# Kernel tuning notes

Hardware: AMD Instinct MI355X
Metric: run time of the kernel (lower is better)

## Reference

```python
import jax, jax.numpy as jnp
import numpy as np

NH = 8          # n_heads
EPS = 1e-12     # layer_norm_eps


def _ln(x, g, b, eps=EPS):
    m = x.mean(-1, keepdims=True)
    v = jnp.var(x, axis=-1, keepdims=True)
    return (x - m) / jnp.sqrt(v + eps) * g + b


def _heads(x):
    # [B,S,H] -> [B,NH,S,H/NH]
    B, S, H = x.shape
    return x.reshape(B, S, NH, H // NH).transpose(0, 2, 1, 3)


def setup_inputs() -> dict:
    B, S, H, INNER = 32, 512, 512, 2048
    n_items = 50000
    std = 0.02
    ks = list(jax.random.split(jax.random.key(0), 20))
    inp = {}
    inp['x'] = jax.random.normal(ks[0], (B, S, H), jnp.float32)
    inp['value_input'] = jax.random.normal(ks[1], (B, S, H), jnp.float32)
    inp['beha_emb'] = jax.random.normal(ks[2], (B, S, H), jnp.float32)
    inp['pos_table'] = std * jax.random.normal(ks[3], (S, H), jnp.float32)
    names = ['q', 'k', 'v', 'pk', 'pq', 'bk', 'bq', 'd']
    for i, n in enumerate(names):
        inp['W' + n] = std * jax.random.normal(ks[4 + i], (H, H), jnp.float32)
        inp['b' + n] = jnp.zeros((H,), jnp.float32)
    inp['ln_g'] = jnp.ones((H,), jnp.float32)
    inp['ln_b'] = jnp.zeros((H,), jnp.float32)
    inp['W1'] = std * jax.random.normal(ks[12], (H, INNER), jnp.float32)
    inp['b1'] = jnp.zeros((INNER,), jnp.float32)
    inp['W2'] = std * jax.random.normal(ks[13], (INNER, H), jnp.float32)
    inp['b2'] = jnp.zeros((H,), jnp.float32)
    inp['ln2_g'] = jnp.ones((H,), jnp.float32)
    inp['ln2_b'] = jnp.zeros((H,), jnp.float32)
    inp['item_seq'] = jax.random.randint(ks[14], (B, S), 0, n_items, jnp.int32)
    return inp


def reference(x, value_input, beha_emb, pos_table, Wq, bq, Wk, bk, Wv, bv,
              Wpk, bpk, Wpq, bpq, Wbk, bbk, Wbq, bbq, Wd, bd, ln_g, ln_b,
              W1, b1, W2, b2, ln2_g, ln2_b, item_seq):
    B, S, H = x.shape
    dh = H // NH
    pos = pos_table[:S][None]  # [1,S,H] position_embedding(arange(S))

    q = _heads(x @ Wq + bq)
    k = _heads(x @ Wk + bk)
    v = _heads(value_input @ Wv + bv + value_input)  # value(value_input) + value_input
    pk = _heads(jnp.broadcast_to(pos @ Wpk + bpk, (B, S, H)))
    pq = _heads(jnp.broadcast_to(pos @ Wpq + bpq, (B, S, H)))
    bhk = _heads(beha_emb @ Wbk + bbk)
    bhq = _heads(beha_emb @ Wbq + bbq)

    # disentangled score: q.k^T + q.((beha_k+pos_k)/2)^T + ((beha_q+pos_q)/2).k^T
    scores = (jnp.einsum('bhqd,bhkd->bhqk', q, k)
              + jnp.einsum('bhqd,bhkd->bhqk', q, (bhk + pk) * 0.5)
              + jnp.einsum('bhqd,bhkd->bhqk', (bhq + pq) * 0.5, k))
    scores = scores / (dh ** 0.5)

    # causal + padding mask: (1 - mask) * -10000
    valid = item_seq > 0                              # [B,S]
    causal = jnp.tril(jnp.ones((S, S), bool))         # [S,S]
    ok = valid[:, None, None, :] & causal[None, None]
    scores = scores + jnp.where(ok, 0.0, -10000.0)

    probs = jax.nn.softmax(scores, axis=-1)
    ctx = jnp.einsum('bhqk,bhkd->bhqd', probs, v)
    ctx = ctx.transpose(0, 2, 1, 3).reshape(B, S, H)

    attn_out = _ln(ctx @ Wd + bd + x, ln_g, ln_b)

    # FeedForward (RecBole): dense1 -> gelu -> dense2 -> LN(residual)
    h = jax.nn.gelu(attn_out @ W1 + b1, approximate=False)
    h = h @ W2 + b2
    return _ln(h + attn_out, ln2_g, ln2_b)
```

## Files before the change

### kernel.cpp

```cpp
#include <hip/hip_runtime.h>
#include <math.h>


typedef unsigned short u16;
typedef __attribute__((ext_vector_type(8))) short bf16x8;
typedef __attribute__((ext_vector_type(4))) float f32x4;

#define NM 16384

__device__ __forceinline__ u16 f2b(float f) {
  union { float f; unsigned u; } x; x.f = f;
  return (u16)((x.u + 0x7fffu + ((x.u >> 16) & 1u)) >> 16);
}
__device__ __forceinline__ float b2f(u16 u) {
  union { unsigned u; float f; } x; x.u = ((unsigned)u) << 16; return x.f;
}
__device__ __forceinline__ f32x4 mfma16(bf16x8 a, bf16x8 b, f32x4 c) {
  return __builtin_amdgcn_mfma_f32_16x16x32_bf16(a, b, c, 0, 0, 0);
}
__device__ __forceinline__ void gl16(const u16* g, u16* l) {
  __builtin_amdgcn_global_load_lds(
      (const __attribute__((address_space(1))) unsigned int*)(const void*)g,
      (__attribute__((address_space(3))) unsigned int*)(void*)l, 16, 0, 0);
}
__device__ __forceinline__ bf16x8 baddv(bf16x8 a, bf16x8 b) {
  bf16x8 r;
  #pragma unroll
  for (int e = 0; e < 8; ++e) r[e] = (short)f2b(b2f((u16)a[e]) + b2f((u16)b[e]));
  return r;
}

__device__ __forceinline__ void kloop(
    const u16* __restrict__ A, const u16* __restrict__ W,
    int m0, int n0, int K, int kiters, u16* As, u16* Bs, bool vres,
    f32x4 (&acc)[4][4])
{
  const int tid = threadIdx.x;
  const int wave = tid>>6, lane = tid&63, quad = lane>>4, l16 = lane&15;
  const int wm = wave>>1, wn = wave&1;
  const int r1 = tid>>2;
  const int ch1 = (((tid&3) ^ ((r1>>1)&3)) << 3);
  const int qsw = ((quad ^ ((l16>>1)&3)) << 3);
  const u16* pA = A + (size_t)(m0+r1)*K + ch1;
  const u16* pB = W + (size_t)(n0+r1)*K + ch1;
  u16* sa = As + tid*8;  u16* sb = Bs + tid*8;
  for (int it = 0; it < kiters; ++it) {
    const int k0 = it*32;
    gl16(pA + k0, sa); gl16(pA + (size_t)64*K + k0, sa + 2048);
    gl16(pB + k0, sb); gl16(pB + (size_t)64*K + k0, sb + 2048);
    __syncthreads();
    bf16x8 af[4], bf[4];
    #pragma unroll
    for (int i = 0; i < 4; ++i)
      af[i] = *(const bf16x8*)&As[(wm*64 + i*16 + l16)*32 + qsw];
    #pragma unroll
    for (int j = 0; j < 4; ++j)
      bf[j] = *(const bf16x8*)&Bs[(wn*64 + j*16 + l16)*32 + qsw];
    if (vres) {
      #pragma unroll
      for (int j = 0; j < 4; ++j) {
        const int start = n0 + wn*64 + j*16;
        if ((start & ~31) == k0) {
          const int c = (start & 31) + l16;
          #pragma unroll
          for (int i = 0; i < 4; ++i)
            #pragma unroll
            for (int rr = 0; rr < 4; ++rr) {
              const int rw = wm*64 + i*16 + quad*4 + rr;
              const int sw = ((((c>>3) ^ ((rw>>1)&3)) << 3) | (c & 7));
              acc[i][j][rr] += b2f(As[rw*32 + sw]);
            }
        }
      }
    }
    #pragma unroll
    for (int i = 0; i < 4; ++i)
      #pragma unroll
      for (int j = 0; j < 4; ++j)
        acc[i][j] = mfma16(af[i], bf[j], acc[i][j]);
    __syncthreads();
  }
}

__device__ __forceinline__ void epi_std(
    f32x4 (&acc)[4][4], const float* __restrict__ bias,
    const u16* __restrict__ ex, int exmode, float scale, int gelu,
    u16* __restrict__ out, int m0, int n0, int N, u16* til)
{
  const int tid = threadIdx.x;
  const int wave = tid>>6, lane = tid&63, quad = lane>>4, l16 = lane&15;
  const int wm = wave>>1, wn = wave&1;
  #pragma unroll
  for (int pass = 0; pass < 2; ++pass) {
    if (wm == pass) {
      #pragma unroll
      for (int j = 0; j < 4; ++j) {
        const int c = wn*64 + j*16 + l16;
        const float bv = bias[n0 + c];
        #pragma unroll
        for (int i = 0; i < 4; ++i)
          #pragma unroll
          for (int rr = 0; rr < 4; ++rr) {
            float v = acc[i][j][rr] + bv;
            if (gelu) v = 0.5f*v*(1.0f + erff(v*0.70710678118654752f));
            til[(i*16 + quad*4 + rr)*136 + c] = f2b(v);
          }
      }
    }
    __syncthreads();
    const int r = tid>>2, ck = tid&3;
    const int gr = m0 + pass*64 + r;
    #pragma unroll
    for (int kk = 0; kk < 4; ++kk) {
      const int cc = ck*32 + kk*8, gc = n0 + cc;
      u16 e8[8];
      *(uint4*)e8 = *(const uint4*)&til[r*136 + cc];
      if (exmode) {
        const u16* ep = (exmode == 1) ? &ex[(size_t)(gr & 511)*512 + gc]
                                      : &ex[(size_t)gr*512 + gc];
        #pragma unroll
        for (int e = 0; e < 8; ++e) e8[e] = f2b((b2f(e8[e]) + b2f(ep[e]))*scale);
      } else if (scale != 1.0f) {
        #pragma unroll
        for (int e = 0; e < 8; ++e) e8[e] = f2b(b2f(e8[e])*scale);
      }
      *(uint4*)&out[(size_t)gr*N + gc] = *(uint4*)e8;
    }
    __syncthreads();
  }
}

__device__ __forceinline__ void epi_vt(
    f32x4 (&acc)[4][4], const float* __restrict__ bias,
    u16* __restrict__ Vt, int m0, int n0, u16* til)
{
  const int tid = threadIdx.x;
  const int wave = tid>>6, lane = tid&63, quad = lane>>4, l16 = lane&15;
  const int wm = wave>>1, wn = wave&1;
  const int b = m0 >> 9, s0 = m0 & 511;
  #pragma unroll
  for (int pass = 0; pass < 2; ++pass) {
    if (wn == pass) {
      #pragma unroll
      for (int j = 0; j < 4; ++j) {
        const int cl = j*16 + l16;
        const float bv = bias[n0 + pass*64 + cl];
        #pragma unroll
        for (int i = 0; i < 4; ++i)
          #pragma unroll
          for (int rr = 0; rr < 4; ++rr)
            til[cl*136 + wm*64 + i*16 + quad*4 + rr] = f2b(acc[i][j][rr] + bv);
      }
    }
    __syncthreads();
    const int cl = tid>>2, ck = tid&3;
    const int gn = n0 + pass*64 + cl, h = gn>>6, d = gn&63;
    u16* orow = Vt + ((size_t)((b*8 + h)*64 + d))*512 + s0 + ck*32;
    #pragma unroll
    for (int kk = 0; kk < 4; ++kk)
      *(uint4*)&orow[kk*8] = *(const uint4*)&til[cl*136 + ck*32 + kk*8];
    __syncthreads();
  }
}

struct PJ { const u16* A; const u16* W; const float* bias; const u16* ex;
            u16* out; float scale; int exmode; int epiv; };
struct ProjArgs { PJ p[7]; };

__global__ __launch_bounds__(256, 2) void proj_kernel(ProjArgs pa, int phaseBase) {
  __shared__ __align__(16) u16 smem[8704];
  u16* As = smem;  u16* Bs = smem + 4096;
  const PJ P = pa.p[phaseBase + (blockIdx.x >> 2)];
  const int n0 = (blockIdx.x & 3)*128, m0 = blockIdx.y*128;
  f32x4 acc[4][4] = {};
  kloop(P.A, P.W, m0, n0, 512, 16, As, Bs, P.epiv != 0, acc);
  if (P.epiv) epi_vt(acc, P.bias, P.out, m0, n0, smem);
  else        epi_std(acc, P.bias, P.ex, P.exmode, P.scale, 0, P.out, m0, n0, 512, smem);
}

template<int GELU>
__global__ __launch_bounds__(256, 2) void gemm1_kernel(
    const u16* __restrict__ A, const u16* __restrict__ W,
    const float* __restrict__ bias, u16* __restrict__ out, int N, int K)
{
  __shared__ __align__(16) u16 smem[8704];
  const int m0 = blockIdx.y*128, n0 = blockIdx.x*128;
  f32x4 acc[4][4] = {};
  kloop(A, W, m0, n0, K, K>>5, smem, smem + 4096, false, acc);
  epi_std(acc, bias, nullptr, 0, 1.0f, GELU, out, m0, n0, N, smem);
}

__global__ __launch_bounds__(256) void cast_all_kernel(
    const float* __restrict__ x, const float* __restrict__ v,
    const float* __restrict__ be, const float* __restrict__ pos,
    u16* __restrict__ xb, u16* __restrict__ vb, u16* __restrict__ bb,
    u16* __restrict__ posb)
{
  int z = blockIdx.y;
  const float* in = (z==0) ? x : (z==1) ? v : (z==2) ? be : pos;
  u16* out = (z==0) ? xb : (z==1) ? vb : (z==2) ? bb : posb;
  int n4 = (z < 3) ? (NM*512/4) : (512*512/4);
  int i = blockIdx.x*256 + threadIdx.x;
  if (i >= n4) return;
  float4 w = ((const float4*)in)[i];
  ((ushort4*)out)[i] = make_ushort4(f2b(w.x), f2b(w.y), f2b(w.z), f2b(w.w));
}

struct PrepArgs {
  const float* w[10];
  u16* o[10];
  const float* bbq; const float* bbk;
  float* Bq2; float* Bk2;
};
__global__ __launch_bounds__(256) void wprep_all_kernel(PrepArgs a) {
  int job = blockIdx.x;
  if (job == 1024) {
    for (int i = threadIdx.x; i < 512; i += 256) {
      a.Bq2[i] = 0.5f*a.bbq[i];
      a.Bk2[i] = 0.5f*a.bbk[i];
    }
    return;
  }
  int wsel, n0, k0, K, N;
  if (job < 512)      { wsel = job>>6; int t = job&63;  n0=(t&7)*64;  k0=(t>>3)*64; K=512;  N=512; }
  else if (job < 768) { wsel = 8;      int t = job-512; n0=(t&31)*64; k0=(t>>5)*64; K=512;  N=2048; }
  else                { wsel = 9;      int t = job-768; n0=(t&7)*64;  k0=(t>>3)*64; K=2048; N=512; }
  float sc = (wsel == 5 || wsel == 6) ? 0.5f : 1.0f;
  const float* in = a.w[wsel];
  u16* out = a.o[wsel];
  __shared__ __align__(16) u16 til[64*72];
  for (int idx = threadIdx.x; idx < 4096; idx += 256) {
    int r = idx>>6, c = idx&63;
    til[r*72+c] = f2b(in[(size_t)(k0+r)*N + n0+c] * sc);
  }
  __syncthreads();
  for (int idx = threadIdx.x; idx < 4096; idx += 256) {
    int r = idx>>6, c = idx&63;
    out[(size_t)(n0+r)*K + k0+c] = til[c*72+r];
  }
}

__global__ __launch_bounds__(512, 2) void attn_kernel(
    const u16* __restrict__ Qraw, const u16* __restrict__ Praw,
    const u16* __restrict__ Kraw, const u16* __restrict__ Mraw,
    const u16* __restrict__ Vt, const int* __restrict__ iseq,
    u16* __restrict__ ctx)
{
  const int qh = blockIdx.x, h = blockIdx.y, b = blockIdx.z;
  const int tid = threadIdx.x;
  const int wave = tid>>6, lane = tid&63, quad = lane>>4, l16 = lane&15;

  __shared__ __align__(16) u16 Ks[2][64*136];
  __shared__ __align__(16) u16 Vs[2][64*72];
  __shared__ __align__(16) u16 Ps[8][16*72];
  __shared__ float sel[512];

  const int q0 = qh*256;
  const int ntiles = 4*qh + 4;
  const u16* Kg = Kraw + (size_t)(b*512)*512 + h*64;
  const u16* Mg = Mraw + (size_t)(b*512)*512 + h*64;
  const u16* Vg = Vt + (size_t)((b*8 + h)*64)*512;

  if (tid < 512) sel[tid] = (iseq[b*512 + tid] > 0) ? 1.0f : 1e-30f;

  bf16x8 aq[2][4];
  #pragma unroll
  for (int s = 0; s < 2; ++s) {
    const size_t ro = (size_t)(b*512 + q0 + s*128 + wave*16 + l16)*512 + h*64;
    bf16x8 qf0 = *(const bf16x8*)&Qraw[ro + quad*8];
    bf16x8 qf1 = *(const bf16x8*)&Qraw[ro + 32 + quad*8];
    bf16x8 pf0 = *(const bf16x8*)&Praw[ro + quad*8];
    bf16x8 pf1 = *(const bf16x8*)&Praw[ro + 32 + quad*8];
    aq[s][0] = baddv(qf0, pf0); aq[s][1] = baddv(qf1, pf1);
    aq[s][2] = qf0;             aq[s][3] = qf1;
  }

  const int sr = tid>>3, sc8 = (tid&7)*8;
  uint4 kreg = *(const uint4*)&Kg[(size_t)sr*512 + sc8];
  uint4 mreg = *(const uint4*)&Mg[(size_t)sr*512 + sc8];
  uint4 vreg = *(const uint4*)&Vg[(size_t)sr*512 + sc8];

  f32x4 Ob[2][4] = {};
  float lrow[2][4] = {};
  u16* Pw = Ps[wave];
  int buf = 0;

  for (int kt = 0; kt < ntiles; ++kt) {
    const int k0 = kt*64;
    *(uint4*)&Ks[buf][sr*136 + sc8]      = kreg;
    *(uint4*)&Ks[buf][sr*136 + 64 + sc8] = mreg;
    *(uint4*)&Vs[buf][sr*72 + sc8]       = vreg;
    __syncthreads();
    if (kt + 1 < ntiles) {
      const int kn = k0 + 64;
      kreg = *(const uint4*)&Kg[(size_t)(kn + sr)*512 + sc8];
      mreg = *(const uint4*)&Mg[(size_t)(kn + sr)*512 + sc8];
      vreg = *(const uint4*)&Vg[(size_t)sr*512 + kn + sc8];
    }
    const bool act0 = (q0 + wave*16 + 15) >= k0;
    const bool act1 = (q0 + 128 + wave*16 + 15) >= k0;
    if (act1) {
      f32x4 sc[2][4] = {};
      #pragma unroll
      for (int ks = 0; ks < 4; ++ks) {
        bf16x8 bk[4];
        #pragma unroll
        for (int j = 0; j < 4; ++j)
          bk[j] = *(const bf16x8*)&Ks[buf][(j*16 + l16)*136 + ks*32 + quad*8];
        if (act0) {
          #pragma unroll
          for (int j = 0; j < 4; ++j) sc[0][j] = mfma16(aq[0][ks], bk[j], sc[0][j]);
        }
        #pragma unroll
        for (int j = 0; j < 4; ++j) sc[1][j] = mfma16(aq[1][ks], bk[j], sc[1][j]);
      }
      #pragma unroll
      for (int s = 0; s < 2; ++s) {
        if (s == 0 && !act0) continue;
        const int rb = q0 + s*128 + wave*16 + quad*4;
        float pj[4][4];
        #pragma unroll
        for (int j = 0; j < 4; ++j) {
          int col = k0 + j*16 + l16;
          float fs = sel[col];
          #pragma unroll
          for (int r = 0; r < 4; ++r) {
            float m2 = (col <= rb + r) ? fs : 1e-30f;
            pj[j][r] = __expf(sc[s][j][r]) * m2;
          }
        }
        #pragma unroll
        for (int r = 0; r < 4; ++r)
          lrow[s][r] += pj[0][r] + pj[1][r] + pj[2][r] + pj[3][r];
        #pragma unroll
        for (int j = 0; j < 4; ++j)
          #pragma unroll
          for (int r = 0; r < 4; ++r)
            Pw[(quad*4 + r)*72 + j*16 + l16] = f2b(pj[j][r]);
        #pragma unroll
        for (int c = 0; c < 4; ++c) {
          #pragma unroll
          for (int k2 = 0; k2 < 2; ++k2) {
            bf16x8 ap = *(const bf16x8*)&Pw[l16*72 + k2*32 + quad*8];
            bf16x8 bv = *(const bf16x8*)&Vs[buf][(c*16 + l16)*72 + k2*32 + quad*8];
            Ob[s][c] = mfma16(ap, bv, Ob[s][c]);
          }
        }
      }
    }
    buf ^= 1;
  }

  #pragma unroll
  for (int s = 0; s < 2; ++s) {
    #pragma unroll
    for (int r = 0; r < 4; ++r) {
      float l = lrow[s][r];
      #pragma unroll
      for (int d2 = 1; d2 < 16; d2 <<= 1) l += __shfl_xor(l, d2, 64);
      float inv = 1.0f / l;
      int grow = b*512 + q0 + s*128 + wave*16 + quad*4 + r;
      #pragma unroll
      for (int c = 0; c < 4; ++c)
        ctx[(size_t)grow*512 + h*64 + c*16 + l16] = f2b(Ob[s][c][r]*inv);
    }
  }
}

template<int RES>
__global__ __launch_bounds__(256) void ln_kernel(
    const u16* __restrict__ a, const void* __restrict__ resv,
    const float* __restrict__ g, const float* __restrict__ be,
    float* __restrict__ of, u16* __restrict__ ob)
{
  const int wave = threadIdx.x >> 6, lane = threadIdx.x & 63;
  const int row = blockIdx.x*4 + wave;
  const ushort4* pa = (const ushort4*)(a + (size_t)row*512);
  ushort4 a0 = pa[lane], a1 = pa[lane+64];
  float v[8] = { b2f(a0.x), b2f(a0.y), b2f(a0.z), b2f(a0.w),
                 b2f(a1.x), b2f(a1.y), b2f(a1.z), b2f(a1.w) };
  if (RES == 1) {
    const ushort4* pr = (const ushort4*)((const u16*)resv + (size_t)row*512);
    ushort4 u0 = pr[lane], u1 = pr[lane+64];
    v[0]+=b2f(u0.x); v[1]+=b2f(u0.y); v[2]+=b2f(u0.z); v[3]+=b2f(u0.w);
    v[4]+=b2f(u1.x); v[5]+=b2f(u1.y); v[6]+=b2f(u1.z); v[7]+=b2f(u1.w);
  } else {
    const float4* pr = (const float4*)((const float*)resv + (size_t)row*512);
    float4 r0 = pr[lane], r1 = pr[lane+64];
    v[0]+=r0.x; v[1]+=r0.y; v[2]+=r0.z; v[3]+=r0.w;
    v[4]+=r1.x; v[5]+=r1.y; v[6]+=r1.z; v[7]+=r1.w;
  }
  float s = 0.f, q = 0.f;
  #pragma unroll
  for (int e = 0; e < 8; ++e) { s += v[e]; q += v[e]*v[e]; }
  #pragma unroll
  for (int d = 1; d < 64; d <<= 1) { s += __shfl_xor(s, d, 64); q += __shfl_xor(q, d, 64); }
  float mean = s * (1.0f/512.0f);
  float var  = q * (1.0f/512.0f) - mean*mean;
  float rstd = rsqrtf(var + 1e-12f);
  float4 g0 = ((const float4*)g)[lane],  g1 = ((const float4*)g)[lane+64];
  float4 b0 = ((const float4*)be)[lane], b1 = ((const float4*)be)[lane+64];
  float o[8];
  o[0]=(v[0]-mean)*rstd*g0.x+b0.x; o[1]=(v[1]-mean)*rstd*g0.y+b0.y;
  o[2]=(v[2]-mean)*rstd*g0.z+b0.z; o[3]=(v[3]-mean)*rstd*g0.w+b0.w;
  o[4]=(v[4]-mean)*rstd*g1.x+b1.x; o[5]=(v[5]-mean)*rstd*g1.y+b1.y;
  o[6]=(v[6]-mean)*rstd*g1.z+b1.z; o[7]=(v[7]-mean)*rstd*g1.w+b1.w;
  if (of) {
    ((float4*)(of + (size_t)row*512))[lane]    = make_float4(o[0],o[1],o[2],o[3]);
    ((float4*)(of + (size_t)row*512))[lane+64] = make_float4(o[4],o[5],o[6],o[7]);
  }
  if (ob) {
    ((ushort4*)(ob + (size_t)row*512))[lane]    = make_ushort4(f2b(o[0]),f2b(o[1]),f2b(o[2]),f2b(o[3]));
    ((ushort4*)(ob + (size_t)row*512))[lane+64] = make_ushort4(f2b(o[4]),f2b(o[5]),f2b(o[6]),f2b(o[7]));
  }
}

extern "C" void kernel_launch(void* const* d_in, const int* in_sizes, int n_in,
                              void* d_out, int out_size, void* d_ws, size_t ws_size,
                              hipStream_t stream) {
  (void)in_sizes; (void)n_in; (void)out_size; (void)ws_size;
  const float* x    = (const float*)d_in[0];
  const float* vin  = (const float*)d_in[1];
  const float* beh  = (const float*)d_in[2];
  const float* pos  = (const float*)d_in[3];
  const float* bq   = (const float*)d_in[5];
  const float* bk   = (const float*)d_in[7];
  const float* bv   = (const float*)d_in[9];
  const float* bpk  = (const float*)d_in[11];
  const float* bpq  = (const float*)d_in[13];
  const float* bbk  = (const float*)d_in[15];
  const float* bbq  = (const float*)d_in[17];
  const float* bd   = (const float*)d_in[19];
  const float* ln_g = (const float*)d_in[20];
  const float* ln_b = (const float*)d_in[21];
  const float* b1   = (const float*)d_in[23];
  const float* b2   = (const float*)d_in[25];
  const float* ln2_g= (const float*)d_in[26];
  const float* ln2_b= (const float*)d_in[27];
  const int*   iseq = (const int*)d_in[28];
  float* out = (float*)d_out;
  char* ws = (char*)d_ws;

  size_t off = 0;
  auto nxt = [&](size_t sz) { size_t r = off; off += (sz + 255) & ~(size_t)255; return r; };
  size_t oWT[8]; for (int i = 0; i < 8; ++i) oWT[i] = nxt(512*512*2);
  size_t oW1T = nxt((size_t)512*2048*2);
  size_t oW2T = nxt((size_t)512*2048*2);
  size_t oBq2 = nxt(512*4);
  size_t oBk2 = nxt(512*4);
  size_t oPb  = nxt(512*512*2);
  size_t oPQ  = nxt(512*512*2);
  size_t oPK  = nxt(512*512*2);
  size_t oXb  = nxt((size_t)NM*512*2);
  size_t oVb  = nxt((size_t)NM*512*2);
  size_t oBb  = nxt((size_t)NM*512*2);
  size_t oQr  = nxt((size_t)NM*512*2);
  size_t oPr  = nxt((size_t)NM*512*2);
  size_t oKr  = nxt((size_t)NM*512*2);
  size_t oMr  = nxt((size_t)NM*512*2);
  size_t oVt  = nxt((size_t)NM*512*2);

  u16* WT[8]; for (int i = 0; i < 8; ++i) WT[i] = (u16*)(ws + oWT[i]);
  u16*   W1T  = (u16*)(ws + oW1T);
  u16*   W2T  = (u16*)(ws + oW2T);
  float* Bq2  = (float*)(ws + oBq2);
  float* Bk2  = (float*)(ws + oBk2);
  u16*   posb = (u16*)(ws + oPb);
  u16*   PQs  = (u16*)(ws + oPQ);
  u16*   PKs  = (u16*)(ws + oPK);
  u16*   xb   = (u16*)(ws + oXb);
  u16*   vb   = (u16*)(ws + oVb);
  u16*   bb   = (u16*)(ws + oBb);
  u16*   Qraw = (u16*)(ws + oQr);
  u16*   Praw = (u16*)(ws + oPr);
  u16*   Kraw = (u16*)(ws + oKr);
  u16*   Mraw = (u16*)(ws + oMr);
  u16*   Vtb  = (u16*)(ws + oVt);
  u16*   Cb   = (u16*)(ws + oVb);
  u16*   db   = (u16*)(ws + oPr);
  u16*   ab   = (u16*)(ws + oXb);
  u16*   h1b  = (u16*)(ws + oQr);
  u16*   f2   = (u16*)(ws + oVt);

  cast_all_kernel<<<dim3(8192, 4), 256, 0, stream>>>(x, vin, beh, pos, xb, vb, bb, posb);
  PrepArgs pr;
  const int wi[10] = {4, 6, 8, 10, 12, 14, 16, 18, 22, 24};
  for (int i = 0; i < 10; ++i) pr.w[i] = (const float*)d_in[wi[i]];
  for (int i = 0; i < 8; ++i)  pr.o[i] = WT[i];
  pr.o[8] = W1T; pr.o[9] = W2T;
  pr.bbq = bbq; pr.bbk = bbk; pr.Bq2 = Bq2; pr.Bk2 = Bk2;
  wprep_all_kernel<<<1025, 256, 0, stream>>>(pr);
  ProjArgs pj;
  pj.p[0] = { xb,   WT[0], bq,   nullptr, Qraw, 0.125f, 0, 0 };
  pj.p[1] = { xb,   WT[1], bk,   nullptr, Kraw, 1.0f,   0, 0 };
  pj.p[2] = { bb,   WT[6], Bq2,  PQs,     Praw, 0.125f, 1, 0 };
  pj.p[3] = { bb,   WT[5], Bk2,  PKs,     Mraw, 1.0f,   1, 0 };
  pj.p[4] = { vb,   WT[2], bv,   nullptr, Vtb,  1.0f,   0, 1 };
  pj.p[5] = { posb, WT[4], bpq,  nullptr, PQs,  0.5f,   0, 0 };
  pj.p[6] = { posb, WT[3], bpk,  nullptr, PKs,  0.5f,   0, 0 };
  proj_kernel<<<dim3(8, 4), 256, 0, stream>>>(pj, 5);
  proj_kernel<<<dim3(20, 128), 256, 0, stream>>>(pj, 0);
  attn_kernel<<<dim3(2, 8, 32), 512, 0, stream>>>(Qraw, Praw, Kraw, Mraw, Vtb, iseq, Cb);
  gemm1_kernel<0><<<dim3(4, 128), 256, 0, stream>>>(Cb, WT[7], bd, db, 512, 512);
  ln_kernel<0><<<4096, 256, 0, stream>>>(db, x, ln_g, ln_b, nullptr, ab);
  gemm1_kernel<1><<<dim3(16, 128), 256, 0, stream>>>(ab, W1T, b1, h1b, 2048, 512);
  gemm1_kernel<0><<<dim3(4, 128), 256, 0, stream>>>(h1b, W2T, b2, f2, 512, 2048);
  ln_kernel<1><<<4096, 256, 0, stream>>>(f2, ab, ln2_g, ln2_b, out, nullptr);
}
```

Baseline: 583.9 us.

## Double-buffer GEMM LDS tiles and remap workgroups across XCDs

```diff
diff --git a/kernel.cpp b/kernel.cpp
--- a/kernel.cpp
+++ b/kernel.cpp
@@ -32,7 +32,7 @@
 
 __device__ __forceinline__ void kloop(
     const u16* __restrict__ A, const u16* __restrict__ W,
-    int m0, int n0, int K, int kiters, u16* As, u16* Bs, bool vres,
+    int m0, int n0, int K, int kiters, u16* sm, bool vres,
     f32x4 (&acc)[4][4])
 {
   const int tid = threadIdx.x;
@@ -43,12 +43,21 @@
   const int qsw = ((quad ^ ((l16>>1)&3)) << 3);
   const u16* pA = A + (size_t)(m0+r1)*K + ch1;
   const u16* pB = W + (size_t)(n0+r1)*K + ch1;
-  u16* sa = As + tid*8;  u16* sb = Bs + tid*8;
+  u16* s0 = sm + tid*8;
+  gl16(pA, s0);              gl16(pA + (size_t)64*K, s0 + 2048);
+  gl16(pB, s0 + 4096);       gl16(pB + (size_t)64*K, s0 + 6144);
+  asm volatile("s_waitcnt vmcnt(0)" ::: "memory");
+  __builtin_amdgcn_s_barrier();
+  int buf = 0;
   for (int it = 0; it < kiters; ++it) {
-    const int k0 = it*32;
-    gl16(pA + k0, sa); gl16(pA + (size_t)64*K + k0, sa + 2048);
-    gl16(pB + k0, sb); gl16(pB + (size_t)64*K + k0, sb + 2048);
-    __syncthreads();
+    if (it + 1 < kiters) {
+      const int kn = (it + 1)*32;
+      u16* sn = s0 + (buf^1)*8192;
+      gl16(pA + kn, sn);           gl16(pA + (size_t)64*K + kn, sn + 2048);
+      gl16(pB + kn, sn + 4096);    gl16(pB + (size_t)64*K + kn, sn + 6144);
+    }
+    const u16* As = sm + buf*8192;
+    const u16* Bs = As + 4096;
     bf16x8 af[4], bf[4];
     #pragma unroll
     for (int i = 0; i < 4; ++i)
@@ -57,6 +66,7 @@
     for (int j = 0; j < 4; ++j)
       bf[j] = *(const bf16x8*)&Bs[(wn*64 + j*16 + l16)*32 + qsw];
     if (vres) {
+      const int k0 = it*32;
       #pragma unroll
       for (int j = 0; j < 4; ++j) {
         const int start = n0 + wn*64 + j*16;
@@ -78,7 +88,9 @@
       #pragma unroll
       for (int j = 0; j < 4; ++j)
         acc[i][j] = mfma16(af[i], bf[j], acc[i][j]);
-    __syncthreads();
+    asm volatile("s_waitcnt vmcnt(0)" ::: "memory");
+    __builtin_amdgcn_s_barrier();
+    buf ^= 1;
   }
 }
 
@@ -168,12 +180,16 @@
 struct ProjArgs { PJ p[7]; };
 
 __global__ __launch_bounds__(256, 2) void proj_kernel(ProjArgs pa, int phaseBase) {
-  __shared__ __align__(16) u16 smem[8704];
-  u16* As = smem;  u16* Bs = smem + 4096;
-  const PJ P = pa.p[phaseBase + (blockIdx.x >> 2)];
-  const int n0 = (blockIdx.x & 3)*128, m0 = blockIdx.y*128;
+  __shared__ __align__(16) u16 smem[16384];
+  const int nbx = gridDim.x;
+  const int nwg = nbx * gridDim.y;
+  int lin = blockIdx.y*nbx + blockIdx.x;
+  lin = (lin & 7)*(nwg >> 3) + (lin >> 3);
+  const int bx = lin % nbx, by = lin / nbx;
+  const PJ P = pa.p[phaseBase + (bx >> 2)];
+  const int n0 = (bx & 3)*128, m0 = by*128;
   f32x4 acc[4][4] = {};
-  kloop(P.A, P.W, m0, n0, 512, 16, As, Bs, P.epiv != 0, acc);
+  kloop(P.A, P.W, m0, n0, 512, 16, smem, P.epiv != 0, acc);
   if (P.epiv) epi_vt(acc, P.bias, P.out, m0, n0, smem);
   else        epi_std(acc, P.bias, P.ex, P.exmode, P.scale, 0, P.out, m0, n0, 512, smem);
 }
@@ -183,10 +199,14 @@
     const u16* __restrict__ A, const u16* __restrict__ W,
     const float* __restrict__ bias, u16* __restrict__ out, int N, int K)
 {
-  __shared__ __align__(16) u16 smem[8704];
-  const int m0 = blockIdx.y*128, n0 = blockIdx.x*128;
+  __shared__ __align__(16) u16 smem[16384];
+  const int nbx = gridDim.x;
+  const int nwg = nbx * gridDim.y;
+  int lin = blockIdx.y*nbx + blockIdx.x;
+  lin = (lin & 7)*(nwg >> 3) + (lin >> 3);
+  const int m0 = (lin / nbx)*128, n0 = (lin % nbx)*128;
   f32x4 acc[4][4] = {};
-  kloop(A, W, m0, n0, K, K>>5, smem, smem + 4096, false, acc);
+  kloop(A, W, m0, n0, K, K>>5, smem, false, acc);
   epi_std(acc, bias, nullptr, 0, 1.0f, GELU, out, m0, n0, N, smem);
 }
 
```

Result: faster. 501.4 us (-14.1%).
